# Optimization experiments

Hardware: AMD Instinct MI355X
Metric: run time of the kernel (lower is better)

## Reference

```python
import jax, jax.numpy as jnp
import numpy as np
from jax import lax

B, N, E, H = 512, 128, 256, 8
D = E // H
CLIP = 10.0
NEG = -1e9  # finite stand-in for -inf (backward-safe, math-identical after softmax)


def setup_inputs() -> dict:
    key = jax.random.key(0)
    ks = jax.random.split(key, 5)
    s = lambda k, shape: jax.random.normal(k, shape, jnp.float32) * 0.05
    return {
        "node_embeddings": jax.random.normal(ks[0], (B, N, E), jnp.float32),
        "Wqkv": s(ks[1], (E, 3 * E)), "bqkv": jnp.zeros((3 * E,), jnp.float32),
        "Wfix": s(ks[2], (E, E)), "bfix": jnp.zeros((E,), jnp.float32),
        "Wstep": s(ks[3], (2 * E, E)), "bstep": jnp.zeros((E,), jnp.float32),
        "Wmlp": s(ks[4], (E, E)), "bmlp": jnp.zeros((E,), jnp.float32),
    }


def reference(node_embeddings, Wqkv, bqkv, Wfix, bfix, Wstep, bstep, Wmlp, bmlp):
    scale = 1.0 / np.sqrt(D)
    graph_emb = node_embeddings.mean(axis=1)                       # (B,E)
    qkv = node_embeddings @ Wqkv + bqkv                            # (B,N,3E)
    k, v, logit_k = jnp.split(qkv, 3, axis=-1)
    kh = k.reshape(B, N, H, D).transpose(0, 2, 1, 3)               # (B,H,N,D)
    vh = v.reshape(B, N, H, D).transpose(0, 2, 1, 3)               # (B,H,N,D)
    fixed = graph_emb @ Wfix + bfix                                # (B,E)
    first = node_embeddings[:, 0, :]                               # (B,E)
    bidx = jnp.arange(B)

    def step(carry, _):
        current, visited, logp_sum = carry
        last = node_embeddings[bidx, current]                      # gather last action emb (B,E)
        q = fixed + (jnp.concatenate([first, last], axis=-1) @ Wstep + bstep)
        qh = q.reshape(B, H, D)                                    # single query per head
        attn = jnp.einsum('bhd,bhnd->bhn', qh, kh) * scale
        attn = jnp.where(visited[:, None, :], NEG, attn)
        attn = jax.nn.softmax(attn, axis=-1)
        ctx = jnp.einsum('bhn,bhnd->bhd', attn, vh).reshape(B, E)
        x = ctx @ Wmlp + bmlp                                      # (B,E)
        logits = jnp.einsum('be,bne->bn', x, logit_k) * scale      # (B,N)
        logits = jnp.tanh(logits) * CLIP
        logits = jnp.where(visited, NEG, logits)
        log_p = jax.nn.log_softmax(logits, axis=-1)
        action = jnp.argmax(log_p, axis=-1)                        # greedy decode
        chosen = jnp.take_along_axis(log_p, action[:, None], axis=1)[:, 0]
        visited = visited | jax.nn.one_hot(action, N, dtype=bool)
        return (action, visited, logp_sum + chosen), action

    visited0 = jnp.zeros((B, N), bool).at[:, 0].set(True)
    current0 = jnp.zeros((B,), jnp.int32)
    (_, _, logp_sum), seq = lax.scan(
        step, (current0, visited0, jnp.zeros((B,), jnp.float32)), None, length=N - 1)
    return logp_sum                                                # (B,) summed log-prob of tour
```

## Files before the change

kernel.cpp:

```cpp
#include <hip/hip_runtime.h>
#include <math.h>


#define B_ 512
#define N_ 128
#define E_ 256
#define H_ 8
#define D_ 32
#define NEG (-1.0e9f)
#define CLIPV 10.0f
#define SCALE 0.17677669529663688110f

template <int CTRL>
__device__ __forceinline__ float dpp_f(float x) {
  int r = __builtin_amdgcn_update_dpp(__float_as_int(x), __float_as_int(x),
                                      CTRL, 0xf, 0xf, false);
  return __int_as_float(r);
}
__device__ __forceinline__ float wred_max(float v) {
  v = fmaxf(v, dpp_f<0xB1>(v));
  v = fmaxf(v, dpp_f<0x4E>(v));
  v = fmaxf(v, dpp_f<0x124>(v));
  v = fmaxf(v, dpp_f<0x128>(v));
  v = fmaxf(v, __shfl_xor(v, 16));
  v = fmaxf(v, __shfl_xor(v, 32));
  return v;
}
__device__ __forceinline__ float wred_sum(float v) {
  v += dpp_f<0xB1>(v);
  v += dpp_f<0x4E>(v);
  v += dpp_f<0x124>(v);
  v += dpp_f<0x128>(v);
  v += __shfl_xor(v, 16);
  v += __shfl_xor(v, 32);
  return v;
}

__global__ void k0_prep(const float* __restrict__ Wqkv, const float* __restrict__ bqkv,
                        const float* __restrict__ Wmlp, const float* __restrict__ bmlp,
                        float* __restrict__ Wc, float* __restrict__ bc,
                        float* __restrict__ wc2, float* __restrict__ cconst) {
  int t = threadIdx.x;
  int blk = blockIdx.x;
  __shared__ float row_s[E_];
  if (blk < E_) {
    int g = blk;
    row_s[t] = Wqkv[g * 768 + 512 + t];
    __syncthreads();
    int f = t;
    const float4* wm4 = (const float4*)(Wmlp + f * E_);
    const float4* w34 = (const float4*)row_s;
    float acc = 0.f;
#pragma unroll 8
    for (int j = 0; j < E_ / 4; ++j) {
      float4 a = w34[j]; float4 bv = wm4[j];
      acc += a.x * bv.x + a.y * bv.y + a.z * bv.z + a.w * bv.w;
    }
    Wc[g * E_ + f] = acc;
  } else {
    int f = t;
    float a1 = 0.f, a2 = 0.f;
    for (int e = 0; e < E_; ++e) {
      a1 += bqkv[512 + e] * Wmlp[f * E_ + e];
      a2 += Wqkv[f * 768 + 512 + e] * bmlp[e];
    }
    bc[f] = a1;
    wc2[f] = a2;
    if (t == 0) {
      float c = 0.f;
      for (int e = 0; e < E_; ++e) c += bqkv[512 + e] * bmlp[e];
      *cconst = c;
    }
  }
}

__global__ __launch_bounds__(256, 2)
void k_gemm(const float* __restrict__ emb, const float* __restrict__ Wqkv,
            const float* __restrict__ bqkv,
            const float* __restrict__ Wc, const float* __restrict__ bc,
            float* __restrict__ kk_, float* __restrict__ vv_,
            float* __restrict__ lk2, int ncc, int tmask) {
  __shared__ float As[256 * 64];
  int t = threadIdx.x;
  int r0 = blockIdx.x * 64;
  {
    int m = t >> 2;
    int c0 = t & 3;
    const float4* e4 = (const float4*)emb;
#pragma unroll
    for (int p = 0; p < 16; ++p) {
      int c4 = c0 + p * 4;
      float4 a = e4[(size_t)(r0 + m) * 64 + c4];
      As[(c4 * 4 + 0) * 64 + m] = a.x;
      As[(c4 * 4 + 1) * 64 + m] = a.y;
      As[(c4 * 4 + 2) * 64 + m] = a.z;
      As[(c4 * 4 + 3) * 64 + m] = a.w;
    }
  }
  __syncthreads();
  int tx = t & 15, ty = t >> 4;
  const float4* As4 = (const float4*)As;
  for (int cc = 0; cc < ncc; ++cc) {
    const float* Bp; int ldb4; const float* bias; float* outp;
    int colbase = (cc & 1) * 128;
    switch (cc >> 1) {
      case 0:  Bp = Wqkv + colbase;          ldb4 = 192; bias = bqkv + colbase;       outp = kk_; break;
      case 1:  Bp = Wqkv + 256 + colbase;    ldb4 = 192; bias = bqkv + 256 + colbase; outp = vv_; break;
      default: Bp = Wc + colbase;            ldb4 = 64;  bias = bc + colbase;         outp = lk2; break;
    }
    const float4* B4 = (const float4*)Bp;
    float acc[4][8];
#pragma unroll
    for (int i = 0; i < 4; ++i)
#pragma unroll
      for (int j = 0; j < 8; ++j) acc[i][j] = 0.f;

#pragma unroll 4
    for (int kk = 0; kk < 256; ++kk) {
      float4 b0 = B4[kk * ldb4 + tx * 2];
      float4 b1 = B4[kk * ldb4 + tx * 2 + 1];
      float4 av = As4[kk * 16 + ty];
      float a_[4] = {av.x, av.y, av.z, av.w};
#pragma unroll
      for (int i = 0; i < 4; ++i) {
        acc[i][0] += a_[i] * b0.x; acc[i][1] += a_[i] * b0.y;
        acc[i][2] += a_[i] * b0.z; acc[i][3] += a_[i] * b0.w;
        acc[i][4] += a_[i] * b1.x; acc[i][5] += a_[i] * b1.y;
        acc[i][6] += a_[i] * b1.z; acc[i][7] += a_[i] * b1.w;
      }
    }
    float bj[8];
#pragma unroll
    for (int j = 0; j < 8; ++j) bj[j] = bias ? bias[tx * 8 + j] : 0.f;
    int tr = (tmask >> (cc >> 1)) & 1;
    if (!tr) {
#pragma unroll
      for (int i = 0; i < 4; ++i) {
        int row = r0 + ty * 4 + i;
        float4 o0 = make_float4(acc[i][0] + bj[0], acc[i][1] + bj[1], acc[i][2] + bj[2], acc[i][3] + bj[3]);
        float4 o1 = make_float4(acc[i][4] + bj[4], acc[i][5] + bj[5], acc[i][6] + bj[6], acc[i][7] + bj[7]);
        float4* o4 = (float4*)(outp + (size_t)row * 256 + colbase + tx * 8);
        o4[0] = o0; o4[1] = o1;
      }
    } else {
#pragma unroll
      for (int i = 0; i < 4; ++i) {
        int row = r0 + ty * 4 + i;
        int bb = row >> 7, nn = row & 127;
        float* op = outp + (size_t)bb * 32768 + nn;
#pragma unroll
        for (int j = 0; j < 8; ++j)
          op[(size_t)(colbase + tx * 8 + j) * 128] = acc[i][j] + bj[j];
      }
    }
  }
}

__global__ void k_qbase(const float* __restrict__ emb, const float* __restrict__ Wfix,
                        const float* __restrict__ bfix, const float* __restrict__ Wstep,
                        const float* __restrict__ bstep, float* __restrict__ qbase) {
  int b = blockIdx.x, t = threadIdx.x;
  __shared__ float ge[E_], fi[E_];
  const float* eb = emb + (size_t)b * N_ * E_;
  float s = 0.f;
#pragma unroll 8
  for (int n = 0; n < N_; ++n) s += eb[n * E_ + t];
  ge[t] = s * (1.0f / 128.0f);
  fi[t] = eb[t];
  __syncthreads();
  float acc = bfix[t] + bstep[t];
#pragma unroll 4
  for (int g = 0; g < E_; ++g)
    acc += ge[g] * Wfix[g * E_ + t] + fi[g] * Wstep[g * E_ + t];
  qbase[b * E_ + t] = acc;
}

__global__ void k_c(const float* __restrict__ emb, const float* __restrict__ wc2,
                    const float* __restrict__ cconst, float* __restrict__ cvec) {
  __shared__ float w[E_];
  int t = threadIdx.x;
  w[t] = wc2[t];
  __syncthreads();
  int row = blockIdx.x * 256 + t;
  const float4* e4 = (const float4*)(emb + (size_t)row * E_);
  const float4* w4 = (const float4*)w;
  float acc = 0.f;
#pragma unroll 8
  for (int j = 0; j < E_ / 4; ++j) {
    float4 a = e4[j], bv = w4[j];
    acc += a.x * bv.x + a.y * bv.y + a.z * bv.z + a.w * bv.w;
  }
  cvec[row] = acc + *cconst;
}

__global__ __launch_bounds__(512, 2)
void k_roll(const float* __restrict__ emb, const float* __restrict__ Wstep,
            const float* __restrict__ kT, const float* __restrict__ vv_,
            const float* __restrict__ lkT,
            const float* __restrict__ qbase, const float* __restrict__ cvec,
            float* __restrict__ out) {
  int lt = threadIdx.x;
  int b = blockIdx.x;
  int h = lt >> 6;
  int j = lt & 63;

  __shared__ float sq_lds[128 * 260];
  __shared__ float work[6144];
  float* at_s  = work;
  float* ctx_s = work + 1024;
  float* zp    = work + 1280;

  {
    float* At = work;
    float* Bs = work + 2048;
    const float4* eb4 = (const float4*)(emb + (size_t)b * 32768);
    const float* W2 = Wstep + 65536;
    int n0 = (lt & 31) * 4;
    int e0 = (lt >> 5) * 16;
    float acc[4][16];
#pragma unroll
    for (int i = 0; i < 4; ++i)
#pragma unroll
      for (int jj = 0; jj < 16; ++jj) acc[i][jj] = 0.f;

    for (int gc = 0; gc < 16; ++gc) {
      {
        int n = lt & 127, q4g = lt >> 7;
        float4 a = eb4[n * 64 + gc * 4 + q4g];
        At[(q4g * 4 + 0) * 128 + n] = a.x;
        At[(q4g * 4 + 1) * 128 + n] = a.y;
        At[(q4g * 4 + 2) * 128 + n] = a.z;
        At[(q4g * 4 + 3) * 128 + n] = a.w;
      }
      {
        const float4* w4 = (const float4*)(W2 + gc * 16 * 256);
        ((float4*)Bs)[lt] = w4[lt];
        ((float4*)Bs)[lt + 512] = w4[lt + 512];
      }
      __syncthreads();
#pragma unroll
      for (int gi = 0; gi < 16; ++gi) {
        float4 a4 = *(const float4*)(At + gi * 128 + n0);
        const float4* bp = (const float4*)(Bs + gi * 256 + e0);
        float4 b0 = bp[0], b1 = bp[1], b2 = bp[2], b3 = bp[3];
        float av[4] = {a4.x, a4.y, a4.z, a4.w};
        float bv[16] = {b0.x, b0.y, b0.z, b0.w, b1.x, b1.y, b1.z, b1.w,
                        b2.x, b2.y, b2.z, b2.w, b3.x, b3.y, b3.z, b3.w};
#pragma unroll
        for (int i = 0; i < 4; ++i)
#pragma unroll
          for (int jj = 0; jj < 16; ++jj) acc[i][jj] += av[i] * bv[jj];
      }
      __syncthreads();
    }
    const float* qb = qbase + (size_t)b * 256;
    float qbr[16];
#pragma unroll
    for (int jj = 0; jj < 16; ++jj) qbr[jj] = qb[e0 + jj];
#pragma unroll
    for (int i = 0; i < 4; ++i)
#pragma unroll
      for (int jj = 0; jj < 16; ++jj)
        sq_lds[(n0 + i) * 260 + e0 + jj] = acc[i][jj] + qbr[jj];
  }
  __syncthreads();
  __builtin_amdgcn_sched_barrier(0);

  const float* kTb = kT + (size_t)b * 32768;
  const float* vb  = vv_ + (size_t)b * 32768;
  const float* lTb = lkT + (size_t)b * 32768;

  float k0r[32], k1r[32];
#pragma unroll
  for (int d = 0; d < 32; ++d) {
    k0r[d] = kTb[(h * 32 + d) * 128 + j];
    k1r[d] = kTb[(h * 32 + d) * 128 + j + 64];
  }
  int e_own = h * 32 + (j & 31), nh = j >> 5;
  float vr[64];
#pragma unroll
  for (int m = 0; m < 64; ++m) vr[m] = vb[(nh * 64 + m) * 256 + e_own];
  float l0r[32], l1r[32];
#pragma unroll
  for (int e = 0; e < 32; ++e) {
    l0r[e] = lTb[(h * 32 + e) * 128 + j];
    l1r[e] = lTb[(h * 32 + e) * 128 + j + 64];
  }
  float cv_lo = cvec[b * 128 + j];
  float cv_hi = cvec[b * 128 + j + 64];
  int vis_lo = (j == 0) ? 1 : 0, vis_hi = 0;
  int cur = 0;
  float lp = 0.f;

#pragma unroll 1
  for (int it = 0; it < N_ - 1; ++it) {
    const float4* q4 = (const float4*)(sq_lds + cur * 260 + h * 32);
    float sa0 = 0.f, sb0 = 0.f, sa1 = 0.f, sb1 = 0.f;
#pragma unroll
    for (int dd = 0; dd < 8; ++dd) {
      float4 qv = q4[dd];
      if (dd & 1) {
        sb0 += qv.x * k0r[dd * 4] + qv.y * k0r[dd * 4 + 1] + qv.z * k0r[dd * 4 + 2] + qv.w * k0r[dd * 4 + 3];
        sb1 += qv.x * k1r[dd * 4] + qv.y * k1r[dd * 4 + 1] + qv.z * k1r[dd * 4 + 2] + qv.w * k1r[dd * 4 + 3];
      } else {
        sa0 += qv.x * k0r[dd * 4] + qv.y * k0r[dd * 4 + 1] + qv.z * k0r[dd * 4 + 2] + qv.w * k0r[dd * 4 + 3];
        sa1 += qv.x * k1r[dd * 4] + qv.y * k1r[dd * 4 + 1] + qv.z * k1r[dd * 4 + 2] + qv.w * k1r[dd * 4 + 3];
      }
    }
    float slo = vis_lo ? NEG : (sa0 + sb0) * SCALE;
    float shi = vis_hi ? NEG : (sa1 + sb1) * SCALE;
    float m = wred_max(fmaxf(slo, shi));
    float elo = expf(slo - m), ehi = expf(shi - m);
    at_s[h * 128 + j] = elo;
    at_s[h * 128 + 64 + j] = ehi;
    float inv = 1.0f / wred_sum(elo + ehi);
    const float4* a4 = (const float4*)(at_s + h * 128 + nh * 64);
    float c0 = 0.f, c1 = 0.f;
#pragma unroll
    for (int mm = 0; mm < 16; ++mm) {
      float4 av = a4[mm];
      if (mm & 1)
        c1 += av.x * vr[mm * 4] + av.y * vr[mm * 4 + 1] + av.z * vr[mm * 4 + 2] + av.w * vr[mm * 4 + 3];
      else
        c0 += av.x * vr[mm * 4] + av.y * vr[mm * 4 + 1] + av.z * vr[mm * 4 + 2] + av.w * vr[mm * 4 + 3];
    }
    float c = c0 + c1;
    c += __shfl_xor(c, 32);
    c *= inv;
    if (j < 32) ctx_s[h * 32 + j] = c;
    const float4* cx4 = (const float4*)(ctx_s + h * 32);
    float z0a = 0.f, z0b = 0.f, z1a = 0.f, z1b = 0.f;
#pragma unroll
    for (int ee = 0; ee < 8; ++ee) {
      float4 cv = cx4[ee];
      if (ee & 1) {
        z0b += cv.x * l0r[ee * 4] + cv.y * l0r[ee * 4 + 1] + cv.z * l0r[ee * 4 + 2] + cv.w * l0r[ee * 4 + 3];
        z1b += cv.x * l1r[ee * 4] + cv.y * l1r[ee * 4 + 1] + cv.z * l1r[ee * 4 + 2] + cv.w * l1r[ee * 4 + 3];
      } else {
        z0a += cv.x * l0r[ee * 4] + cv.y * l0r[ee * 4 + 1] + cv.z * l0r[ee * 4 + 2] + cv.w * l0r[ee * 4 + 3];
        z1a += cv.x * l1r[ee * 4] + cv.y * l1r[ee * 4 + 1] + cv.z * l1r[ee * 4 + 2] + cv.w * l1r[ee * 4 + 3];
      }
    }
    float* zpw = zp + (it & 1) * 1024;
    zpw[h * 128 + j] = z0a + z0b;
    zpw[h * 128 + 64 + j] = z1a + z1b;
    __syncthreads();

    float zlo = cv_lo, zhi = cv_hi;
#pragma unroll
    for (int hh = 0; hh < 8; ++hh) {
      zlo += zpw[hh * 128 + j];
      zhi += zpw[hh * 128 + 64 + j];
    }
    float zmlo = vis_lo ? -1e30f : zlo;
    float zmhi = vis_hi ? -1e30f : zhi;
    float vmax = wred_max(fmaxf(zmlo, zmhi));
    unsigned long long blo = __ballot(zmlo == vmax);
    int action;
    if (blo) action = __ffsll((unsigned long long)blo) - 1;
    else     action = 63 + __ffsll((unsigned long long)__ballot(zmhi == vmax));
    float lmax = CLIPV * tanhf(vmax * SCALE);
    float tlo = vis_lo ? 0.f : expf(CLIPV * tanhf(zlo * SCALE) - 10.0f);
    float thi = vis_hi ? 0.f : expf(CLIPV * tanhf(zhi * SCALE) - 10.0f);
    float S = wred_sum(tlo + thi);
    lp += lmax - 10.0f - logf(S);
    cur = action;
    vis_lo |= (action == j);
    vis_hi |= (action == j + 64);
  }
  if (lt == 0) out[b] = lp;
}

extern "C" void kernel_launch(void* const* d_in, const int* in_sizes, int n_in,
                              void* d_out, int out_size, void* d_ws, size_t ws_size,
                              hipStream_t stream) {
  (void)in_sizes; (void)n_in; (void)out_size; (void)ws_size;
  const float* emb   = (const float*)d_in[0];
  const float* Wqkv  = (const float*)d_in[1];
  const float* bqkv  = (const float*)d_in[2];
  const float* Wfix  = (const float*)d_in[3];
  const float* bfix  = (const float*)d_in[4];
  const float* Wstep = (const float*)d_in[5];
  const float* bstep = (const float*)d_in[6];
  const float* Wmlp  = (const float*)d_in[7];
  const float* bmlp  = (const float*)d_in[8];
  float* out = (float*)d_out;
  float* ws = (float*)d_ws;

  const size_t NBE = (size_t)B_ * N_ * E_;
  float* kk_    = ws;
  float* vv_    = ws + NBE;
  float* lk2    = ws + 2 * NBE;
  float* qbase  = ws + 3 * NBE;
  float* cvec   = qbase + 131072;
  float* Wc     = cvec + 65536;
  float* bc     = Wc + 65536;
  float* wc2    = bc + 256;
  float* cconst = wc2 + 256;

  hipLaunchKernelGGL(k0_prep, dim3(257), dim3(256), 0, stream,
                     Wqkv, bqkv, Wmlp, bmlp, Wc, bc, wc2, cconst);
  hipLaunchKernelGGL(k_qbase, dim3(512), dim3(256), 0, stream,
                     emb, Wfix, bfix, Wstep, bstep, qbase);
  hipLaunchKernelGGL(k_c, dim3(256), dim3(256), 0, stream,
                     emb, wc2, cconst, cvec);
  hipLaunchKernelGGL(k_gemm, dim3(1024), dim3(256), 0, stream,
                     emb, Wqkv, bqkv, Wc, bc, kk_, vv_, lk2, 6, 0b101);
  hipLaunchKernelGGL(k_roll, dim3(512), dim3(512), 0, stream,
                     emb, Wstep, kk_, vv_, lk2, qbase, cvec, out);
}
```

Before: 1.373 ms.

## Switch k/logit_k to row-major and v to transposed layout for float4 register loads

Changes the k_gemm transpose mask so K and logit-K are stored row-major and V transposed. The rollout kernel can then load its per-thread register operands with contiguous float4 reads instead of strided scalar loads. The loads are expressed as macro-expanded named float4 registers rather than arrays, and the setup GEMM accumulators and stores are vectorized the same way. The sched_barrier is removed. The per-iteration loop is unchanged, so this mainly targets the one-time register fill and compiler register allocation.

```diff
diff --git a/kernel.cpp b/kernel.cpp
--- a/kernel.cpp
+++ b/kernel.cpp
@@ -10,6 +10,17 @@
 #define NEG (-1.0e9f)
 #define CLIPV 10.0f
 #define SCALE 0.17677669529663688110f
+
+#define REP8(M) M(0) M(1) M(2) M(3) M(4) M(5) M(6) M(7)
+#define REP16(M) REP8(M) M(8) M(9) M(10) M(11) M(12) M(13) M(14) M(15)
+#define DOT4(a,b) ((a).x*(b).x + (a).y*(b).y + (a).z*(b).z + (a).w*(b).w)
+
+__device__ __forceinline__ void fma4(float4& d, float a, float4 b) {
+  d.x += a * b.x; d.y += a * b.y; d.z += a * b.z; d.w += a * b.w;
+}
+__device__ __forceinline__ float4 add4(float4 a, float4 b) {
+  return make_float4(a.x + b.x, a.y + b.y, a.z + b.z, a.w + b.w);
+}
 
 template <int CTRL>
 __device__ __forceinline__ float dpp_f(float x) {
@@ -195,8 +206,8 @@
 
 __global__ __launch_bounds__(512, 2)
 void k_roll(const float* __restrict__ emb, const float* __restrict__ Wstep,
-            const float* __restrict__ kT, const float* __restrict__ vv_,
-            const float* __restrict__ lkT,
+            const float* __restrict__ kk, const float* __restrict__ vT,
+            const float* __restrict__ lk,
             const float* __restrict__ qbase, const float* __restrict__ cvec,
             float* __restrict__ out) {
   int lt = threadIdx.x;
@@ -217,11 +228,9 @@
     const float* W2 = Wstep + 65536;
     int n0 = (lt & 31) * 4;
     int e0 = (lt >> 5) * 16;
-    float acc[4][16];
-#pragma unroll
-    for (int i = 0; i < 4; ++i)
-#pragma unroll
-      for (int jj = 0; jj < 16; ++jj) acc[i][jj] = 0.f;
+    float4 z4 = make_float4(0.f, 0.f, 0.f, 0.f);
+#define DECAC(i) float4 ac##i##_0=z4, ac##i##_1=z4, ac##i##_2=z4, ac##i##_3=z4;
+    DECAC(0) DECAC(1) DECAC(2) DECAC(3)
 
     for (int gc = 0; gc < 16; ++gc) {
       {
@@ -240,52 +249,40 @@
       __syncthreads();
 #pragma unroll
       for (int gi = 0; gi < 16; ++gi) {
-        float4 a4 = *(const float4*)(At + gi * 128 + n0);
+        float4 a4v = *(const float4*)(At + gi * 128 + n0);
         const float4* bp = (const float4*)(Bs + gi * 256 + e0);
         float4 b0 = bp[0], b1 = bp[1], b2 = bp[2], b3 = bp[3];
-        float av[4] = {a4.x, a4.y, a4.z, a4.w};
-        float bv[16] = {b0.x, b0.y, b0.z, b0.w, b1.x, b1.y, b1.z, b1.w,
-                        b2.x, b2.y, b2.z, b2.w, b3.x, b3.y, b3.z, b3.w};
-#pragma unroll
-        for (int i = 0; i < 4; ++i)
-#pragma unroll
-          for (int jj = 0; jj < 16; ++jj) acc[i][jj] += av[i] * bv[jj];
+#define ACU(i, comp) fma4(ac##i##_0, a4v.comp, b0); fma4(ac##i##_1, a4v.comp, b1); \
+                     fma4(ac##i##_2, a4v.comp, b2); fma4(ac##i##_3, a4v.comp, b3);
+        ACU(0, x) ACU(1, y) ACU(2, z) ACU(3, w)
       }
       __syncthreads();
     }
-    const float* qb = qbase + (size_t)b * 256;
-    float qbr[16];
-#pragma unroll
-    for (int jj = 0; jj < 16; ++jj) qbr[jj] = qb[e0 + jj];
-#pragma unroll
-    for (int i = 0; i < 4; ++i)
-#pragma unroll
-      for (int jj = 0; jj < 16; ++jj)
-        sq_lds[(n0 + i) * 260 + e0 + jj] = acc[i][jj] + qbr[jj];
+    const float4* qb4 = (const float4*)(qbase + (size_t)b * 256 + e0);
+    float4 qb0 = qb4[0], qb1 = qb4[1], qb2 = qb4[2], qb3 = qb4[3];
+#define STO(i) \
+    *(float4*)(sq_lds + (n0 + (i)) * 260 + e0 + 0)  = add4(ac##i##_0, qb0); \
+    *(float4*)(sq_lds + (n0 + (i)) * 260 + e0 + 4)  = add4(ac##i##_1, qb1); \
+    *(float4*)(sq_lds + (n0 + (i)) * 260 + e0 + 8)  = add4(ac##i##_2, qb2); \
+    *(float4*)(sq_lds + (n0 + (i)) * 260 + e0 + 12) = add4(ac##i##_3, qb3);
+    STO(0) STO(1) STO(2) STO(3)
   }
   __syncthreads();
-  __builtin_amdgcn_sched_barrier(0);
-
-  const float* kTb = kT + (size_t)b * 32768;
-  const float* vb  = vv_ + (size_t)b * 32768;
-  const float* lTb = lkT + (size_t)b * 32768;
-
-  float k0r[32], k1r[32];
-#pragma unroll
-  for (int d = 0; d < 32; ++d) {
-    k0r[d] = kTb[(h * 32 + d) * 128 + j];
-    k1r[d] = kTb[(h * 32 + d) * 128 + j + 64];
-  }
+
+  const float4* kb4 = (const float4*)(kk + (size_t)b * 32768);
+  const float4* vb4 = (const float4*)(vT + (size_t)b * 32768);
+  const float4* lb4 = (const float4*)(lk + (size_t)b * 32768);
   int e_own = h * 32 + (j & 31), nh = j >> 5;
-  float vr[64];
-#pragma unroll
-  for (int m = 0; m < 64; ++m) vr[m] = vb[(nh * 64 + m) * 256 + e_own];
-  float l0r[32], l1r[32];
-#pragma unroll
-  for (int e = 0; e < 32; ++e) {
-    l0r[e] = lTb[(h * 32 + e) * 128 + j];
-    l1r[e] = lTb[(h * 32 + e) * 128 + j + 64];
-  }
+  int row0 = j * 64 + h * 8;
+  int row1 = (j + 64) * 64 + h * 8;
+  int vrow = e_own * 32 + nh * 16;
+
+#define DKL(i) float4 K0_##i = kb4[row0 + (i)], K1_##i = kb4[row1 + (i)], \
+                      L0_##i = lb4[row0 + (i)], L1_##i = lb4[row1 + (i)];
+  REP8(DKL)
+#define DV(i) float4 V_##i = vb4[vrow + (i)];
+  REP16(DV)
+
   float cv_lo = cvec[b * 128 + j];
   float cv_hi = cvec[b * 128 + j + 64];
   int vis_lo = (j == 0) ? 1 : 0, vis_hi = 0;
@@ -296,17 +293,10 @@
   for (int it = 0; it < N_ - 1; ++it) {
     const float4* q4 = (const float4*)(sq_lds + cur * 260 + h * 32);
     float sa0 = 0.f, sb0 = 0.f, sa1 = 0.f, sb1 = 0.f;
-#pragma unroll
-    for (int dd = 0; dd < 8; ++dd) {
-      float4 qv = q4[dd];
-      if (dd & 1) {
-        sb0 += qv.x * k0r[dd * 4] + qv.y * k0r[dd * 4 + 1] + qv.z * k0r[dd * 4 + 2] + qv.w * k0r[dd * 4 + 3];
-        sb1 += qv.x * k1r[dd * 4] + qv.y * k1r[dd * 4 + 1] + qv.z * k1r[dd * 4 + 2] + qv.w * k1r[dd * 4 + 3];
-      } else {
-        sa0 += qv.x * k0r[dd * 4] + qv.y * k0r[dd * 4 + 1] + qv.z * k0r[dd * 4 + 2] + qv.w * k0r[dd * 4 + 3];
-        sa1 += qv.x * k1r[dd * 4] + qv.y * k1r[dd * 4 + 1] + qv.z * k1r[dd * 4 + 2] + qv.w * k1r[dd * 4 + 3];
-      }
-    }
+#define SCM(i) { float4 qv = q4[(i)]; \
+      if ((i) & 1) { sb0 += DOT4(qv, K0_##i); sb1 += DOT4(qv, K1_##i); } \
+      else         { sa0 += DOT4(qv, K0_##i); sa1 += DOT4(qv, K1_##i); } }
+    REP8(SCM)
     float slo = vis_lo ? NEG : (sa0 + sb0) * SCALE;
     float shi = vis_hi ? NEG : (sa1 + sb1) * SCALE;
     float m = wred_max(fmaxf(slo, shi));
@@ -316,31 +306,19 @@
     float inv = 1.0f / wred_sum(elo + ehi);
     const float4* a4 = (const float4*)(at_s + h * 128 + nh * 64);
     float c0 = 0.f, c1 = 0.f;
-#pragma unroll
-    for (int mm = 0; mm < 16; ++mm) {
-      float4 av = a4[mm];
-      if (mm & 1)
-        c1 += av.x * vr[mm * 4] + av.y * vr[mm * 4 + 1] + av.z * vr[mm * 4 + 2] + av.w * vr[mm * 4 + 3];
-      else
-        c0 += av.x * vr[mm * 4] + av.y * vr[mm * 4 + 1] + av.z * vr[mm * 4 + 2] + av.w * vr[mm * 4 + 3];
-    }
+#define CTM(i) { float4 av = a4[(i)]; \
+      if ((i) & 1) c1 += DOT4(av, V_##i); else c0 += DOT4(av, V_##i); }
+    REP16(CTM)
     float c = c0 + c1;
     c += __shfl_xor(c, 32);
     c *= inv;
     if (j < 32) ctx_s[h * 32 + j] = c;
     const float4* cx4 = (const float4*)(ctx_s + h * 32);
     float z0a = 0.f, z0b = 0.f, z1a = 0.f, z1b = 0.f;
-#pragma unroll
-    for (int ee = 0; ee < 8; ++ee) {
-      float4 cv = cx4[ee];
-      if (ee & 1) {
-        z0b += cv.x * l0r[ee * 4] + cv.y * l0r[ee * 4 + 1] + cv.z * l0r[ee * 4 + 2] + cv.w * l0r[ee * 4 + 3];
-        z1b += cv.x * l1r[ee * 4] + cv.y * l1r[ee * 4 + 1] + cv.z * l1r[ee * 4 + 2] + cv.w * l1r[ee * 4 + 3];
-      } else {
-        z0a += cv.x * l0r[ee * 4] + cv.y * l0r[ee * 4 + 1] + cv.z * l0r[ee * 4 + 2] + cv.w * l0r[ee * 4 + 3];
-        z1a += cv.x * l1r[ee * 4] + cv.y * l1r[ee * 4 + 1] + cv.z * l1r[ee * 4 + 2] + cv.w * l1r[ee * 4 + 3];
-      }
-    }
+#define ZPM(i) { float4 cv = cx4[(i)]; \
+      if ((i) & 1) { z0b += DOT4(cv, L0_##i); z1b += DOT4(cv, L1_##i); } \
+      else         { z0a += DOT4(cv, L0_##i); z1a += DOT4(cv, L1_##i); } }
+    REP8(ZPM)
     float* zpw = zp + (it & 1) * 1024;
     zpw[h * 128 + j] = z0a + z0b;
     zpw[h * 128 + 64 + j] = z1a + z1b;
@@ -405,7 +383,7 @@
   hipLaunchKernelGGL(k_c, dim3(256), dim3(256), 0, stream,
                      emb, wc2, cconst, cvec);
   hipLaunchKernelGGL(k_gemm, dim3(1024), dim3(256), 0, stream,
-                     emb, Wqkv, bqkv, Wc, bc, kk_, vv_, lk2, 6, 0b101);
+                     emb, Wqkv, bqkv, Wc, bc, kk_, vv_, lk2, 6, 0b010);
   hipLaunchKernelGGL(k_roll, dim3(512), dim3(512), 0, stream,
                      emb, Wstep, kk_, vv_, lk2, qbase, cvec, out);
 }
```

New measurement: 1.439 ms. 1.05x slower.
